# Optimization experiments

Measured on AMD Instinct MI355X. Metric: run time of the kernel, lower is better.

Reference implementation:

```python
import jax, jax.numpy as jnp
import numpy as np

N_HEAD = 16
N_EMBD = 2048
HEAD_DIM = N_EMBD // N_HEAD
ROPE_BASE = 10000.0


def _rope_cos_sin(seq_len, dim, dtype):
    inv_freq = 1.0 / (ROPE_BASE ** (jnp.arange(0, dim, 2, dtype=jnp.float32) / dim))
    pos = jnp.arange(seq_len, dtype=jnp.float32)
    freqs = jnp.outer(pos, inv_freq)                 # [T, dim/2]
    emb = jnp.concatenate([freqs, freqs], axis=-1)   # [T, dim]
    return jnp.cos(emb).astype(dtype), jnp.sin(emb).astype(dtype)


def _rotate_half(x):
    x1, x2 = jnp.split(x, 2, axis=-1)
    return jnp.concatenate([-x2, x1], axis=-1)


def _apply_rotary(x, cos, sin):
    # x: [B, H, T, D]; cos/sin: [T, D] broadcast over B,H
    return x * cos[None, None] + _rotate_half(x) * sin[None, None]


def setup_inputs() -> dict:
    key = jax.random.key(0)
    ks = jax.random.split(key, 5)
    B, T, C = 4, 2048, N_EMBD
    s_in = 1.0 / np.sqrt(C)
    return {
        "x": jax.random.normal(ks[0], (B, T, C), dtype=jnp.float32),
        "W_attn": jax.random.normal(ks[1], (C, 3 * C), dtype=jnp.float32) * s_in,
        "b_attn": jax.random.normal(ks[2], (3 * C,), dtype=jnp.float32) * 0.02,
        "W_proj": jax.random.normal(ks[3], (C, C), dtype=jnp.float32) * s_in,
        "b_proj": jax.random.normal(ks[4], (C,), dtype=jnp.float32) * 0.02,
    }


def reference(x, W_attn, b_attn, W_proj, b_proj):
    B, T, C = x.shape
    H, D = N_HEAD, HEAD_DIM
    qkv = x @ W_attn + b_attn                        # [B, T, 3C]
    q, k, v = jnp.split(qkv, 3, axis=2)
    q = q.reshape(B, T, H, D).transpose(0, 2, 1, 3)  # [B, H, T, D]
    k = k.reshape(B, T, H, D).transpose(0, 2, 1, 3)
    v = v.reshape(B, T, H, D).transpose(0, 2, 1, 3)

    cos, sin = _rope_cos_sin(T, D, x.dtype)
    q = _apply_rotary(q, cos, sin)
    k = _apply_rotary(k, cos, sin)

    scale = 1.0 / jnp.sqrt(jnp.asarray(D, dtype=x.dtype))
    scores = jnp.einsum('bhqd,bhkd->bhqk', q, k) * scale
    causal = jnp.tril(jnp.ones((T, T), dtype=bool))
    scores = jnp.where(causal[None, None], scores, jnp.finfo(x.dtype).min)
    attn = jax.nn.softmax(scores, axis=-1)
    y = jnp.einsum('bhqk,bhkd->bhqd', attn, v)       # [B, H, T, D]
    y = y.transpose(0, 2, 1, 3).reshape(B, T, C)
    out = y @ W_proj + b_proj                        # dropout p=0 (eval)
    return out, k, v
```

## Files before the change

kernel.cpp:

```cpp
#include <hip/hip_runtime.h>


typedef __attribute__((ext_vector_type(4))) float f32x4;
typedef __attribute__((ext_vector_type(8))) __bf16 bf16x8;
typedef __attribute__((ext_vector_type(4))) unsigned short us4;
typedef __attribute__((ext_vector_type(8))) unsigned short us8;

__device__ __forceinline__ unsigned short f2bf(float f) {
  unsigned u = __float_as_uint(f);
  u += 0x7FFFu + ((u >> 16) & 1u);
  return (unsigned short)(u >> 16);
}

__device__ __forceinline__ void gl_lds16(const void* g, void* l) {
  __builtin_amdgcn_global_load_lds(
      (const __attribute__((address_space(1))) void*)g,
      (__attribute__((address_space(3))) void*)l, 16, 0, 0);
}

__device__ __forceinline__ f32x4 mfma_bf16(bf16x8 a, bf16x8 b, f32x4 c) {
  return __builtin_amdgcn_mfma_f32_16x16x32_bf16(a, b, c, 0, 0, 0);
}


__global__ __launch_bounds__(256) void rope_table_kernel(float* __restrict__ cos_t,
                                                         float* __restrict__ sin_t) {
  int idx = blockIdx.x * 256 + threadIdx.x;
  int t = idx >> 6, i = idx & 63;
  float freq = __expf(-(float)i * 0.14391156831212787f);
  float ang = (float)t * freq;
  float s, c;
  sincosf(ang, &s, &c);
  cos_t[idx] = c;
  sin_t[idx] = s;
}

__global__ __launch_bounds__(256) void conv_bf16_kernel(const float* __restrict__ in,
                                                        unsigned short* __restrict__ out,
                                                        int n4) {
  int idx = blockIdx.x * 256 + threadIdx.x;
  int stride = gridDim.x * 256;
  for (; idx < n4; idx += stride) {
    float4 v = ((const float4*)in)[idx];
    us4 o;
    o[0] = f2bf(v.x); o[1] = f2bf(v.y); o[2] = f2bf(v.z); o[3] = f2bf(v.w);
    ((us4*)out)[idx] = o;
  }
}

__global__ __launch_bounds__(256) void transpose_conv_kernel(const float* __restrict__ in,
                                                             unsigned short* __restrict__ out,
                                                             int R, int C, int permute) {
  __shared__ unsigned short tile[64][68];
  const int t = threadIdx.x;
  const int c0 = blockIdx.x * 64, r0 = blockIdx.y * 64;
  const int cq = t & 15, rr = t >> 4;
#pragma unroll
  for (int i = 0; i < 4; ++i) {
    int r = rr + i * 16;
    float4 v = *(const float4*)&in[(size_t)(r0 + r) * C + c0 + cq * 4];
    tile[r][cq * 4 + 0] = f2bf(v.x);
    tile[r][cq * 4 + 1] = f2bf(v.y);
    tile[r][cq * 4 + 2] = f2bf(v.z);
    tile[r][cq * 4 + 3] = f2bf(v.w);
  }
  __syncthreads();
#pragma unroll
  for (int ii = 0; ii < 4; ++ii) {
    int c = rr + ii * 16;
    int n = c0 + c;
    int np = n;
    if (permute && n < 4096) {
      int d = n & 127, blk = d >> 5;
      int dd = (blk == 1) ? d + 32 : (blk == 2) ? d - 32 : d;
      np = (n & ~127) | dd;
    }
    us4 o;
#pragma unroll
    for (int jj = 0; jj < 4; ++jj) o[jj] = tile[cq * 4 + jj][c];
    *(us4*)&out[(size_t)np * R + r0 + cq * 4] = o;
  }
}


#define BARR __builtin_amdgcn_s_barrier()
#define LGKM                                                                   \
  do {                                                                         \
    asm volatile("s_waitcnt lgkmcnt(0)" ::: "memory");                         \
    __builtin_amdgcn_sched_barrier(0);                                         \
  } while (0)
#define WAITV(N) asm volatile("s_waitcnt vmcnt(" #N ")" ::: "memory")

#define STAGE_A_HALF(BUF, T, H)                                                \
  do {                                                                         \
    const int k0_ = (T) * 64;                                                  \
    _Pragma("unroll") for (int i_ = 0; i_ < 2; ++i_) {                         \
      int c_ = i_ * 512 + tid;                                                 \
      int rp_ = c_ >> 3, s_ = c_ & 7;                                          \
      int row_ = (rp_ & 63) + (H) * 64 + (rp_ >> 6) * 128;                     \
      gl_lds16(Ag + (size_t)row_ * 2048 + k0_ + ((s_ ^ (row_ & 7)) << 3),      \
               &As[BUF][row_ * 64 + s_ * 8]);                                  \
    }                                                                          \
  } while (0)

#define STAGE_B_HALF(BUF, T, H)                                                \
  do {                                                                         \
    const int k0_ = (T) * 64;                                                  \
    _Pragma("unroll") for (int i_ = 0; i_ < 2; ++i_) {                         \
      int c_ = i_ * 512 + tid;                                                 \
      int rp_ = c_ >> 3, s_ = c_ & 7;                                          \
      int row_ = (rp_ & 31) + (H) * 32 + (rp_ >> 5) * 64;                      \
      gl_lds16(Bg + (size_t)row_ * 2048 + k0_ + ((s_ ^ (row_ & 7)) << 3),      \
               &Bs[BUF][row_ * 64 + s_ * 8]);                                  \
    }                                                                          \
  } while (0)

#define LDA(mh)                                                                \
  _Pragma("unroll") for (int m2_ = 0; m2_ < 4; ++m2_)                          \
  _Pragma("unroll") for (int kk_ = 0; kk_ < 2; ++kk_) {                        \
    int R_ = wm * 128 + (mh) * 64 + m2_ * 16 + ln;                             \
    av[m2_][kk_] = *(const bf16x8*)&Ab[R_ * 64 +                               \
        (((kk_ * 64 + g * 16) ^ ((R_ & 7) << 4)) >> 1)];                       \
  }

#define LDB2                                                                   \
  _Pragma("unroll") for (int nh_ = 0; nh_ < 2; ++nh_)                          \
  _Pragma("unroll") for (int n2_ = 0; n2_ < 2; ++n2_)                          \
  _Pragma("unroll") for (int kk_ = 0; kk_ < 2; ++kk_) {                        \
    int R_ = wn * 64 + nh_ * 32 + n2_ * 16 + ln;                               \
    bv[nh_ * 2 + n2_][kk_] = *(const bf16x8*)&Bb[R_ * 64 +                     \
        (((kk_ * 64 + g * 16) ^ ((R_ & 7) << 4)) >> 1)];                       \
  }

#define MF16(mh, nh)                                                           \
  do {                                                                         \
    __builtin_amdgcn_s_setprio(1);                                             \
    _Pragma("unroll") for (int m2_ = 0; m2_ < 4; ++m2_)                        \
    _Pragma("unroll") for (int n2_ = 0; n2_ < 2; ++n2_)                        \
    _Pragma("unroll") for (int kk_ = 0; kk_ < 2; ++kk_)                        \
      acc[(mh) * 4 + m2_][(nh) * 2 + n2_] = mfma_bf16(                         \
          av[m2_][kk_], bv[(nh) * 2 + n2_][kk_],                               \
          acc[(mh) * 4 + m2_][(nh) * 2 + n2_]);                                \
    __builtin_amdgcn_s_setprio(0);                                             \
  } while (0)

#define GEMM_ENGINE_4PH(NT)                                                    \
  STAGE_A_HALF(0, 0, 0); STAGE_B_HALF(0, 0, 0);                                \
  STAGE_B_HALF(0, 0, 1); STAGE_A_HALF(0, 0, 1);                                \
  for (int t = 0; t < (NT); ++t) {                                             \
    const int p_ = t & 1, q_ = p_ ^ 1;                                         \
    const unsigned short* Ab = &As[p_][0];                                     \
    const unsigned short* Bb = &Bs[p_][0];                                     \
    const bool pf_ = (t + 1 < (NT));                                           \
    WAITV(2);                                                                  \
    BARR;                                                                      \
                                \
    LDB2; LDA(0);                                                              \
    if (pf_) STAGE_A_HALF(q_, t + 1, 0);                                       \
    LGKM;                                                                      \
    MF16(0, 0);                                                                \
                                             \
    if (pf_) STAGE_B_HALF(q_, t + 1, 0);                                       \
    MF16(0, 1);                                                                \
    if (pf_) { WAITV(4); } else { WAITV(0); }                                  \
    BARR;                                                                      \
                                        \
    LDA(1);                                                                    \
    if (pf_) STAGE_B_HALF(q_, t + 1, 1);                                       \
    LGKM;                                                                      \
    MF16(1, 0);                                                                \
                                             \
    if (pf_) STAGE_A_HALF(q_, t + 1, 1);                                       \
    MF16(1, 1);                                                                \
  }

__global__ __launch_bounds__(512, 2) void gemm_qkv_kernel(
    const unsigned short* __restrict__ xbf, const unsigned short* __restrict__ wt,
    const float* __restrict__ bias, const float* __restrict__ cost,
    const float* __restrict__ sint, float* __restrict__ out_k,
    float* __restrict__ out_v, unsigned short* __restrict__ qbf,
    unsigned short* __restrict__ kbf, unsigned short* __restrict__ vtb) {
  __shared__ __attribute__((aligned(16))) unsigned short As[2][256 * 64];
  __shared__ __attribute__((aligned(16))) unsigned short Bs[2][256 * 64];
  const int tid = threadIdx.x;
  const int wid = tid >> 6, l = tid & 63, g = l >> 4, ln = l & 15;
  const int wm = wid >> 2, wn = wid & 3;
  const int xcd = blockIdx.x & 7, local = blockIdx.x >> 3;
  const int mtile = xcd * 4 + (local & 3);
  const int ntile = local >> 2;
  const unsigned short* Ag = xbf + (size_t)(mtile * 256) * 2048;
  const unsigned short* Bg = wt + (size_t)(ntile * 256) * 2048;

  f32x4 acc[8][4];
#pragma unroll
  for (int i = 0; i < 8; ++i)
#pragma unroll
    for (int j = 0; j < 4; ++j) acc[i][j] = (f32x4){0.f, 0.f, 0.f, 0.f};
  bf16x8 av[4][2], bv[4][2];

  GEMM_ENGINE_4PH(32);

  const int colb = ntile * 256 + wn * 64;
  const int p = colb >> 11;
  const int h = (colb >> 7) & 15;
  const int Mb = mtile * 256 + wm * 128;

  if (p == 2) {
    __syncthreads();
    unsigned short* reg = (wid < 4) ? &As[0][0] + wid * 8192
                                    : &Bs[0][0] + (wid - 4) * 8192;
    float bvv[4];
#pragma unroll
    for (int nf = 0; nf < 4; ++nf) bvv[nf] = bias[colb + nf * 16 + ln];
    const int dbase = (wn & 1) * 64;
#pragma unroll
    for (int mf = 0; mf < 8; ++mf) {
      int t0 = Mb + mf * 16 + g * 4;
      int bb = t0 >> 11, tt = t0 & 2047;
      size_t base = ((size_t)(bb * 16 + h) * 2048 + tt) * 128;
#pragma unroll
      for (int nf = 0; nf < 4; ++nf) {
        int dl = nf * 16 + ln;
        us4 pack;
#pragma unroll
        for (int r = 0; r < 4; ++r) {
          float val = acc[mf][nf][r] + bvv[nf];
          out_v[base + (size_t)r * 128 + dbase + dl] = val;
          pack[r] = f2bf(val);
        }
        int byt = (mf * 32 + g * 8) ^ ((dl & 7) << 4);
        *(us4*)&reg[dl * 128 + (byt >> 1)] = pack;
      }
    }
    asm volatile("s_waitcnt lgkmcnt(0)" ::: "memory");
    __builtin_amdgcn_sched_barrier(0);
    const size_t vtz = (size_t)((Mb >> 11) * 16 + h) * (128 * 2048);
    const int tbase = (Mb & 2047);
#pragma unroll
    for (int it = 0; it < 16; ++it) {
      int dl = it * 4 + (l >> 4);
      int byt = ((l & 15) * 16) ^ ((dl & 7) << 4);
      us8 v8 = *(const us8*)&reg[dl * 128 + (byt >> 1)];
      *(us8*)&vtb[vtz + (size_t)(dbase + dl) * 2048 + tbase + (l & 15) * 8] = v8;
    }
  } else {
    const float sc2 = 0.12751743681128098f;
    const int half32 = (wn & 1) * 32;
    float blo[2], bhi[2];
#pragma unroll
    for (int nf = 0; nf < 2; ++nf) {
      int d_lo = half32 + nf * 16 + ln;
      blo[nf] = bias[p * 2048 + h * 128 + d_lo];
      bhi[nf] = bias[p * 2048 + h * 128 + d_lo + 64];
    }
#pragma unroll
    for (int mf = 0; mf < 8; ++mf)
#pragma unroll
      for (int r = 0; r < 4; ++r) {
        int m = Mb + mf * 16 + g * 4 + r;
        int b = m >> 11, t = m & 2047;
        size_t base = ((size_t)(b * 16 + h) * 2048 + t) * 128;
#pragma unroll
        for (int nf = 0; nf < 2; ++nf) {
          int d_lo = half32 + nf * 16 + ln;
          float cv = cost[t * 64 + d_lo], sv = sint[t * 64 + d_lo];
          float a = acc[mf][nf][r] + blo[nf];
          float bq = acc[mf][nf + 2][r] + bhi[nf];
          float lo = a * cv - bq * sv;
          float hi = bq * cv + a * sv;
          if (p == 0) {
            qbf[base + d_lo] = f2bf(lo * sc2);
            qbf[base + d_lo + 64] = f2bf(hi * sc2);
          } else {
            out_k[base + d_lo] = lo;
            out_k[base + d_lo + 64] = hi;
            kbf[base + d_lo] = f2bf(lo);
            kbf[base + d_lo + 64] = f2bf(hi);
          }
        }
      }
  }
}

__global__ __launch_bounds__(512, 2) void gemm_proj_kernel(
    const unsigned short* __restrict__ ybf, const unsigned short* __restrict__ wpt,
    const float* __restrict__ bias, float* __restrict__ out) {
  __shared__ __attribute__((aligned(16))) unsigned short As[2][256 * 64];
  __shared__ __attribute__((aligned(16))) unsigned short Bs[2][256 * 64];
  const int tid = threadIdx.x;
  const int wid = tid >> 6, l = tid & 63, g = l >> 4, ln = l & 15;
  const int wm = wid >> 2, wn = wid & 3;
  const int xcd = blockIdx.x & 7, local = blockIdx.x >> 3;
  const int mtile = xcd * 4 + (local & 3);
  const int ntile = local >> 2;
  const unsigned short* Ag = ybf + (size_t)(mtile * 256) * 2048;
  const unsigned short* Bg = wpt + (size_t)(ntile * 256) * 2048;

  f32x4 acc[8][4];
#pragma unroll
  for (int i = 0; i < 8; ++i)
#pragma unroll
    for (int j = 0; j < 4; ++j) acc[i][j] = (f32x4){0.f, 0.f, 0.f, 0.f};
  bf16x8 av[4][2], bv[4][2];

  GEMM_ENGINE_4PH(32);

  const int n0 = ntile * 256 + wn * 64;
  const int Mb = mtile * 256 + wm * 128;
  float bvv[4];
#pragma unroll
  for (int nf = 0; nf < 4; ++nf) bvv[nf] = bias[n0 + nf * 16 + ln];
#pragma unroll
  for (int mf = 0; mf < 8; ++mf)
#pragma unroll
    for (int r = 0; r < 4; ++r) {
      int m = Mb + mf * 16 + g * 4 + r;
      size_t rb = (size_t)m * 2048 + n0;
#pragma unroll
      for (int nf = 0; nf < 4; ++nf)
        out[rb + nf * 16 + ln] = acc[mf][nf][r] + bvv[nf];
    }
}

__global__ __launch_bounds__(256, 2) void attn_kernel(
    const unsigned short* __restrict__ qbf, const unsigned short* __restrict__ kbf,
    const unsigned short* __restrict__ vtbf, unsigned short* __restrict__ ybf) {
  __shared__ __attribute__((aligned(16))) unsigned short Ks[2][64 * 128];
  __shared__ __attribute__((aligned(16))) unsigned short Vs[2][128 * 64];
  __shared__ __attribute__((aligned(16))) __bf16 Ps[4][32 * 64];
  const int tid = threadIdx.x;
  const int w = tid >> 6, l = tid & 63, g = l >> 4, ln = l & 15;
  const int bid = blockIdx.x;
  const int z = (bid & 7) * 8 + ((bid >> 3) & 7);
  const int qp = 15 - (bid >> 6);
  const size_t zo = (size_t)z * (2048 * 128);
  const size_t zv = (size_t)z * (128 * 2048);
  const int Q0w = qp * 128 + w * 32;
  const int jn = 2 * qp + 2;
  const int jlw = 2 * qp + (w >> 1);
  __bf16* Pw = Ps[w];

  bf16x8 qv[2][4];
#pragma unroll
  for (int mf = 0; mf < 2; ++mf)
#pragma unroll
    for (int kk = 0; kk < 4; ++kk)
      qv[mf][kk] = *(const bf16x8*)
          &qbf[zo + (size_t)(Q0w + mf * 16 + ln) * 128 + kk * 32 + g * 8];

  f32x4 o[2][8];
#pragma unroll
  for (int mf = 0; mf < 2; ++mf)
#pragma unroll
    for (int nf = 0; nf < 8; ++nf) o[mf][nf] = (f32x4){0.f, 0.f, 0.f, 0.f};
  float mrun[2][4], lpart[2][4];
#pragma unroll
  for (int mf = 0; mf < 2; ++mf)
#pragma unroll
    for (int r = 0; r < 4; ++r) { mrun[mf][r] = -3e38f; lpart[mf][r] = 0.f; }

#define STAGE_KV(J, B)                                                         \
  do {                                                                         \
    const int kv0_ = (J) << 6;                                                 \
    _Pragma("unroll") for (int i_ = 0; i_ < 4; ++i_) {                         \
      int c_ = i_ * 256 + tid;                                                 \
      int r_ = c_ >> 4, s_ = c_ & 15;                                          \
      gl_lds16(kbf + zo + (size_t)(kv0_ + r_) * 128 +                          \
                   (((s_ * 16) ^ ((r_ & 7) << 4)) >> 1),                       \
               &Ks[B][c_ * 8]);                                                \
    }                                                                          \
    _Pragma("unroll") for (int i_ = 0; i_ < 4; ++i_) {                         \
      int c_ = i_ * 256 + tid;                                                 \
      int d_ = c_ >> 3, s_ = c_ & 7;                                           \
      gl_lds16(vtbf + zv + (size_t)d_ * 2048 + kv0_ +                          \
                   (((s_ * 16) ^ ((d_ & 7) << 4)) >> 1),                       \
               &Vs[B][c_ * 8]);                                                \
    }                                                                          \
  } while (0)

  STAGE_KV(0, 0);
  STAGE_KV(1, 1);

  for (int j = 0; j < jn; ++j) {
    if (j + 1 < jn)
      asm volatile("s_waitcnt vmcnt(8)" ::: "memory");
    else
      asm volatile("s_waitcnt vmcnt(0)" ::: "memory");
    __builtin_amdgcn_s_barrier();
    const int bfr = j & 1;
    const unsigned short* Kb = Ks[bfr];
    const unsigned short* Vb = Vs[bfr];

    if (j <= jlw) {
      const int kv0 = j << 6;
      f32x4 s[2][4];
#pragma unroll
      for (int mf = 0; mf < 2; ++mf)
#pragma unroll
        for (int nf = 0; nf < 4; ++nf) s[mf][nf] = (f32x4){0.f, 0.f, 0.f, 0.f};
#pragma unroll
      for (int kk = 0; kk < 4; ++kk) {
        bf16x8 kf[4];
#pragma unroll
        for (int nf = 0; nf < 4; ++nf) {
          int rr = nf * 16 + ln;
          kf[nf] = *(const bf16x8*)
              &Kb[rr * 128 + (((kk * 64 + g * 16) ^ ((rr & 7) << 4)) >> 1)];
        }
#pragma unroll
        for (int mf = 0; mf < 2; ++mf)
#pragma unroll
          for (int nf = 0; nf < 4; ++nf)
            s[mf][nf] = mfma_bf16(qv[mf][kk], kf[nf], s[mf][nf]);
      }

      if (j == jlw) {
#pragma unroll
        for (int mf = 0; mf < 2; ++mf)
#pragma unroll
          for (int nf = 0; nf < 4; ++nf)
#pragma unroll
            for (int r = 0; r < 4; ++r)
              if (kv0 + nf * 16 + ln > Q0w + mf * 16 + g * 4 + r)
                s[mf][nf][r] = -3e38f;
      }

      float mxl[2][4];
#pragma unroll
      for (int mf = 0; mf < 2; ++mf)
#pragma unroll
        for (int r = 0; r < 4; ++r)
          mxl[mf][r] = fmaxf(fmaxf(s[mf][0][r], s[mf][1][r]),
                             fmaxf(s[mf][2][r], s[mf][3][r]));

      float dm = 0.f;
#pragma unroll
      for (int mf = 0; mf < 2; ++mf)
#pragma unroll
        for (int r = 0; r < 4; ++r) dm = fmaxf(dm, mxl[mf][r] - mrun[mf][r]);
      if (__any(dm > 11.5416f)) {
#pragma unroll
        for (int mf = 0; mf < 2; ++mf)
#pragma unroll
          for (int r = 0; r < 4; ++r) {
            float m0 = mxl[mf][r];
            m0 = fmaxf(m0, __shfl_xor(m0, 1));
            m0 = fmaxf(m0, __shfl_xor(m0, 2));
            m0 = fmaxf(m0, __shfl_xor(m0, 4));
            m0 = fmaxf(m0, __shfl_xor(m0, 8));
            float mn = fmaxf(mrun[mf][r], m0);
            float al = exp2f(mrun[mf][r] - mn);
            mrun[mf][r] = mn;
            lpart[mf][r] *= al;
#pragma unroll
            for (int nf = 0; nf < 8; ++nf) o[mf][nf][r] *= al;
          }
      }

#pragma unroll
      for (int mf = 0; mf < 2; ++mf)
#pragma unroll
        for (int r = 0; r < 4; ++r) {
          const float m0 = mrun[mf][r];
          const int row_l = mf * 16 + g * 4 + r;
          float rs = 0.f;
#pragma unroll
          for (int nf = 0; nf < 4; ++nf) {
            float pv = exp2f(s[mf][nf][r] - m0);
            rs += pv;
            int byte = ((nf * 16 + ln) << 1) ^ ((row_l & 7) << 4);
            Pw[row_l * 64 + (byte >> 1)] = (__bf16)pv;
          }
          lpart[mf][r] += rs;
        }

      asm volatile("s_waitcnt lgkmcnt(0)" ::: "memory");
      __builtin_amdgcn_sched_barrier(0);

#pragma unroll
      for (int kk2 = 0; kk2 < 2; ++kk2) {
        bf16x8 pa[2];
#pragma unroll
        for (int mf = 0; mf < 2; ++mf) {
          int pr = mf * 16 + ln;
          int byte = (kk2 * 64 + g * 16) ^ ((pr & 7) << 4);
          pa[mf] = *(const bf16x8*)&Pw[pr * 64 + (byte >> 1)];
        }
#pragma unroll
        for (int nf2 = 0; nf2 < 8; ++nf2) {
          int dr = nf2 * 16 + ln;
          bf16x8 vf = *(const bf16x8*)
              &Vb[dr * 64 + (((kk2 * 64 + g * 16) ^ ((dr & 7) << 4)) >> 1)];
#pragma unroll
          for (int mf = 0; mf < 2; ++mf)
            o[mf][nf2] = mfma_bf16(pa[mf], vf, o[mf][nf2]);
        }
      }
    }

    __builtin_amdgcn_s_barrier();
    __builtin_amdgcn_sched_barrier(0);
    if (j + 2 < jn) STAGE_KV(j + 2, bfr);
  }
#undef STAGE_KV

  const int b = z >> 4, h = z & 15;
#pragma unroll
  for (int mf = 0; mf < 2; ++mf)
#pragma unroll
    for (int r = 0; r < 4; ++r) {
      float rs = lpart[mf][r];
      rs += __shfl_xor(rs, 1);
      rs += __shfl_xor(rs, 2);
      rs += __shfl_xor(rs, 4);
      rs += __shfl_xor(rs, 8);
      float inv = 1.f / rs;
      int t = Q0w + mf * 16 + g * 4 + r;
      size_t rb = ((size_t)b * 2048 + t) * 2048 + h * 128;
#pragma unroll
      for (int nf2 = 0; nf2 < 8; ++nf2)
        ybf[rb + nf2 * 16 + ln] = f2bf(o[mf][nf2][r] * inv);
    }
}

extern "C" void kernel_launch(void* const* d_in, const int* in_sizes, int n_in,
                              void* d_out, int out_size, void* d_ws, size_t ws_size,
                              hipStream_t stream) {
  (void)in_sizes; (void)n_in; (void)out_size; (void)ws_size;
  const float* x      = (const float*)d_in[0];
  const float* W_attn = (const float*)d_in[1];
  const float* b_attn = (const float*)d_in[2];
  const float* W_proj = (const float*)d_in[3];
  const float* b_proj = (const float*)d_in[4];

  float* out   = (float*)d_out;
  float* out_k = out + 16777216;
  float* out_v = out + 33554432;

  char* ws = (char*)d_ws;
  unsigned short* q_bf  = (unsigned short*)(ws + 0);
  unsigned short* k_bf  = (unsigned short*)(ws + 33554432);
  unsigned short* vt_bf = (unsigned short*)(ws + 67108864);
  unsigned short* x_bf  = (unsigned short*)(ws + 100663296);
  unsigned short* y2d   = x_bf;
  unsigned short* wt    = (unsigned short*)(ws + 134217728);
  unsigned short* wpt   = (unsigned short*)(ws + 159383552);
  float* cos_t = (float*)(ws + 167772160);
  float* sin_t = (float*)(ws + 168296448);

  rope_table_kernel<<<512, 256, 0, stream>>>(cos_t, sin_t);
  conv_bf16_kernel<<<2048, 256, 0, stream>>>(x, x_bf, 16777216 / 4);
  transpose_conv_kernel<<<dim3(6144 / 64, 2048 / 64), 256, 0, stream>>>(W_attn, wt, 2048, 6144, 1);
  transpose_conv_kernel<<<dim3(2048 / 64, 2048 / 64), 256, 0, stream>>>(W_proj, wpt, 2048, 2048, 0);
  gemm_qkv_kernel<<<768, 512, 0, stream>>>(x_bf, wt, b_attn, cos_t, sin_t,
                                           out_k, out_v, q_bf, k_bf, vt_bf);
  attn_kernel<<<1024, 256, 0, stream>>>(q_bf, k_bf, vt_bf, y2d);
  gemm_proj_kernel<<<256, 512, 0, stream>>>(y2d, wpt, b_proj, out);
}
```

Baseline: 427.4 us.

## Fuse prep kernels into one launch and drop explicit LDS waits in QKV GEMM

```diff
diff --git a/kernel.cpp b/kernel.cpp
--- a/kernel.cpp
+++ b/kernel.cpp
@@ -22,38 +22,50 @@
   return __builtin_amdgcn_mfma_f32_16x16x32_bf16(a, b, c, 0, 0, 0);
 }
 
-
-__global__ __launch_bounds__(256) void rope_table_kernel(float* __restrict__ cos_t,
-                                                         float* __restrict__ sin_t) {
-  int idx = blockIdx.x * 256 + threadIdx.x;
-  int t = idx >> 6, i = idx & 63;
-  float freq = __expf(-(float)i * 0.14391156831212787f);
-  float ang = (float)t * freq;
-  float s, c;
-  sincosf(ang, &s, &c);
-  cos_t[idx] = c;
-  sin_t[idx] = s;
-}
-
-__global__ __launch_bounds__(256) void conv_bf16_kernel(const float* __restrict__ in,
-                                                        unsigned short* __restrict__ out,
-                                                        int n4) {
-  int idx = blockIdx.x * 256 + threadIdx.x;
-  int stride = gridDim.x * 256;
-  for (; idx < n4; idx += stride) {
-    float4 v = ((const float4*)in)[idx];
-    us4 o;
-    o[0] = f2bf(v.x); o[1] = f2bf(v.y); o[2] = f2bf(v.z); o[3] = f2bf(v.w);
-    ((us4*)out)[idx] = o;
-  }
-}
-
-__global__ __launch_bounds__(256) void transpose_conv_kernel(const float* __restrict__ in,
-                                                             unsigned short* __restrict__ out,
-                                                             int R, int C, int permute) {
+__global__ __launch_bounds__(256) void prep_kernel(
+    const float* __restrict__ x, unsigned short* __restrict__ x_bf,
+    const float* __restrict__ W_attn, unsigned short* __restrict__ wt,
+    const float* __restrict__ W_proj, unsigned short* __restrict__ wpt,
+    float* __restrict__ cos_t, float* __restrict__ sin_t) {
   __shared__ unsigned short tile[64][68];
+  const int bid = blockIdx.x;
   const int t = threadIdx.x;
-  const int c0 = blockIdx.x * 64, r0 = blockIdx.y * 64;
+
+  if (bid < 2048) {
+    int idx = bid * 256 + t;
+    for (; idx < 4194304; idx += 2048 * 256) {
+      float4 v = ((const float4*)x)[idx];
+      us4 o;
+      o[0] = f2bf(v.x); o[1] = f2bf(v.y); o[2] = f2bf(v.z); o[3] = f2bf(v.w);
+      ((us4*)x_bf)[idx] = o;
+    }
+    return;
+  }
+
+  const float* in;
+  unsigned short* out;
+  int R, C, permute, bx, by;
+  if (bid < 5120) {
+    int loc = bid - 2048;
+    in = W_attn; out = wt; R = 2048; C = 6144; permute = 1;
+    bx = loc % 96; by = loc / 96;
+  } else if (bid < 6144) {
+    int loc = bid - 5120;
+    in = W_proj; out = wpt; R = 2048; C = 2048; permute = 0;
+    bx = loc & 31; by = loc >> 5;
+  } else {
+    int idx = (bid - 6144) * 256 + t;
+    int tt = idx >> 6, i = idx & 63;
+    float freq = __expf(-(float)i * 0.14391156831212787f);
+    float ang = (float)tt * freq;
+    float s, c;
+    sincosf(ang, &s, &c);
+    cos_t[idx] = c;
+    sin_t[idx] = s;
+    return;
+  }
+
+  const int c0 = bx * 64, r0 = by * 64;
   const int cq = t & 15, rr = t >> 4;
 #pragma unroll
   for (int i = 0; i < 4; ++i) {
@@ -84,11 +96,6 @@
 
 
 #define BARR __builtin_amdgcn_s_barrier()
-#define LGKM                                                                   \
-  do {                                                                         \
-    asm volatile("s_waitcnt lgkmcnt(0)" ::: "memory");                         \
-    __builtin_amdgcn_sched_barrier(0);                                         \
-  } while (0)
 #define WAITV(N) asm volatile("s_waitcnt vmcnt(" #N ")" ::: "memory")
 
 #define STAGE_A_HALF(BUF, T, H)                                                \
@@ -154,12 +161,11 @@
     const bool pf_ = (t + 1 < (NT));                                           \
     WAITV(2);                                                                  \
     BARR;                                                                      \
-                                \
+       \
     LDB2; LDA(0);                                                              \
     if (pf_) STAGE_A_HALF(q_, t + 1, 0);                                       \
-    LGKM;                                                                      \
     MF16(0, 0);                                                                \
-                                             \
+                                                       \
     if (pf_) STAGE_B_HALF(q_, t + 1, 0);                                       \
     MF16(0, 1);                                                                \
     if (pf_) { WAITV(4); } else { WAITV(0); }                                  \
@@ -167,9 +173,8 @@
                                         \
     LDA(1);                                                                    \
     if (pf_) STAGE_B_HALF(q_, t + 1, 1);                                       \
-    LGKM;                                                                      \
     MF16(1, 0);                                                                \
-                                             \
+                                                       \
     if (pf_) STAGE_A_HALF(q_, t + 1, 1);                                       \
     MF16(1, 1);                                                                \
   }
@@ -548,10 +553,8 @@
   float* cos_t = (float*)(ws + 167772160);
   float* sin_t = (float*)(ws + 168296448);
 
-  rope_table_kernel<<<512, 256, 0, stream>>>(cos_t, sin_t);
-  conv_bf16_kernel<<<2048, 256, 0, stream>>>(x, x_bf, 16777216 / 4);
-  transpose_conv_kernel<<<dim3(6144 / 64, 2048 / 64), 256, 0, stream>>>(W_attn, wt, 2048, 6144, 1);
-  transpose_conv_kernel<<<dim3(2048 / 64, 2048 / 64), 256, 0, stream>>>(W_proj, wpt, 2048, 2048, 0);
+  prep_kernel<<<6656, 256, 0, stream>>>(x, x_bf, W_attn, wt, W_proj, wpt,
+                                        cos_t, sin_t);
   gemm_qkv_kernel<<<768, 512, 0, stream>>>(x_bf, wt, b_attn, cos_t, sin_t,
                                            out_k, out_v, q_bf, k_bf, vt_bf);
   attn_kernel<<<1024, 256, 0, stream>>>(q_bf, k_bf, vt_bf, y2d);
```

Result: faster. 413.7 us (-3.2%).
